# Optimization experiments

Measured on AMD Instinct MI355X. Metric: run time of the kernel, lower is better.

The kernel has to match this reference:

```python
import jax, jax.numpy as jnp
import numpy as np
from jax import lax

# ---- custom-numeric primitives matching the torch Function classes ----

def _sign1(x):
    # torch.sign with sign(0) -> 1
    return jnp.where(x >= 0, jnp.ones_like(x), -jnp.ones_like(x))

bin_act = _sign1            # BinaryActivation.forward
bin_weight = _sign1         # WeightsToBinary.forward
round_bias = jnp.round      # BiasToInt.forward

C_IN, C_OUT, K = 14, 128, 7
H_MID = 2 * K               # h = k * 2 = 14
PAD = K // 2                # 3


def _conv(x, w, b, stride, pad, groups):
    y = lax.conv_general_dilated(
        x, w,
        window_strides=(stride, stride),
        padding=((pad, pad), (pad, pad)),
        dimension_numbers=("NCHW", "OIHW", "NCHW"),
        feature_group_count=groups,
    )
    return y + b[None, :, None, None]


def setup_inputs() -> dict:
    key = jax.random.key(0)
    ks = jax.random.split(key, 7)
    B, H, W = 8, 384, 384
    x = jax.random.normal(ks[0], (B, C_IN, H, W), dtype=jnp.float32)
    # latent float weights in roughly (-1, 1) like a trained BNN
    w1 = 0.5 * jax.random.normal(ks[1], (H_MID, 1, K, K), dtype=jnp.float32)      # depthwise, groups=C_IN
    b1 = 0.5 * jax.random.normal(ks[2], (H_MID,), dtype=jnp.float32)
    w2 = 0.5 * jax.random.normal(ks[3], (C_OUT, H_MID, 1, 1), dtype=jnp.float32)
    b2 = 0.5 * jax.random.normal(ks[4], (C_OUT,), dtype=jnp.float32)
    w3 = 0.5 * jax.random.normal(ks[5], (C_OUT, C_OUT, 1, 1), dtype=jnp.float32)
    b3 = 0.5 * jax.random.normal(ks[6], (C_OUT,), dtype=jnp.float32)
    return {"x": x, "w1": w1, "b1": b1, "w2": w2, "b2": b2, "w3": w3, "b3": b3}


def reference(x, w1, b1, w2, b2, w3, b3):
    # first=True: center then binarize input
    x = bin_act(x - jnp.mean(x))
    # conv1: depthwise k x k, stride 1, padding k//2 (same spatial)
    y = bin_act(_conv(x, bin_weight(w1), round_bias(b1), 1, PAD, C_IN))
    # conv2: 1x1 conv but padding k//2 (grows spatial by 2*PAD) -- quirk of source
    y = bin_act(_conv(y, bin_weight(w2), round_bias(b2), 1, PAD, 1))
    # conv3: 1x1 conv, stride 3, padding 1
    y = bin_act(_conv(y, bin_weight(w3), round_bias(b3), 3, 1, 1))
    return y
```

## Files before the change

### kernel.cpp

```cpp
#include <hip/hip_runtime.h>
#include <hip/hip_bf16.h>

#define NB     8
#define CIN    14
#define COUT   128
#define HW     384
#define OUT_HW 131
#define P      (OUT_HW*OUT_HW)
#define ROWS   390
#define NTOT   (NB*CIN*HW*HW)
#define NROWS  (NB*CIN*ROWS)
#define NPACK  1024
#define CAND_B 0.002f
#define NSLOT  8
#define NPAIR  66

typedef unsigned long long u64;
typedef unsigned int u32;

struct PackedW {
    uint4 padz;
    uint4 ringz;
    u64   w1pack[CIN];
    int   b1i[CIN];
};

__global__ __launch_bounds__(256) void pass1(
    const float* __restrict__ x, u64* __restrict__ xbin,
    double* __restrict__ part, u64* __restrict__ cands, u32* __restrict__ ccnt,
    const float* __restrict__ w1, const float* __restrict__ b1,
    const float* __restrict__ w2, const float* __restrict__ b2,
    const float* __restrict__ w3, const float* __restrict__ b3,
    uint4* __restrict__ zlut, PackedW* __restrict__ pw)
{
    const int tid  = threadIdx.x;
    const int lane = tid & 63;
    const int wv   = tid >> 6;

    if (blockIdx.x < NPACK) {
        const u64 lmlt = (1ull << lane) - 1ull;
        double s0 = 0.0, s1 = 0.0;
        const int wid = blockIdx.x * 4 + wv;
        for (int row = wid; row < NROWS; row += NPACK * 4) {
            int nc = row / ROWS;
            int rr = row - nc * ROWS;
            int r  = rr - 3;
            u64 v = 0;
            u32 running = 0;
            u64* crow = cands + (size_t)row * NSLOT;
            if (r >= 0 && r < HW) {
                const float* xr = x + ((size_t)nc * HW + r) * HW;
                float f0 = __builtin_nontemporal_load(xr + lane);
                float f1 = __builtin_nontemporal_load(xr + 64 + lane);
                float f2 = __builtin_nontemporal_load(xr + 128 + lane);
                float f3 = __builtin_nontemporal_load(xr + 192 + lane);
                float f4 = __builtin_nontemporal_load(xr + 256 + lane);
                float f5 = __builtin_nontemporal_load(xr + 320 + lane);
                s0 += ((double)f0 + (double)f1) + (double)f2;
                s1 += ((double)f3 + (double)f4) + (double)f5;
                u64 b0 = __ballot(f0 >= 0.f);
                u64 b1_ = __ballot(f1 >= 0.f);
                u64 b2_ = __ballot(f2 >= 0.f);
                u64 b3_ = __ballot(f3 >= 0.f);
                u64 b4_ = __ballot(f4 >= 0.f);
                u64 b5_ = __ballot(f5 >= 0.f);
                v = lane == 0 ? b0 : lane == 1 ? b1_ : lane == 2 ? b2_ :
                    lane == 3 ? b3_ : lane == 4 ? b4_ : lane == 5 ? b5_ : 0;

                const u32 pbase = (u32)row * 512u + (u32)lane;
                float fq[6] = {f0, f1, f2, f3, f4, f5};
                #pragma unroll
                for (int q = 0; q < 6; q++) {
                    u64 cq = __ballot(__builtin_fabsf(fq[q]) < CAND_B);
                    if (cq) {
                        if (__builtin_fabsf(fq[q]) < CAND_B) {
                            u32 slot = running + (u32)__popcll(cq & lmlt);
                            if (slot < NSLOT)
                                crow[slot] = ((u64)__float_as_uint(fq[q]) << 32)
                                           | (pbase + (u32)q * 64u);
                        }
                        running += (u32)__popcll(cq);
                    }
                }
            }
            if (lane < 8) xbin[(size_t)row * 8 + lane] = (lane < 6) ? v : 0;
            if (lane == 0) ccnt[row] = (running > NSLOT) ? NSLOT : running;
        }
        double s = s0 + s1;
        for (int off = 32; off; off >>= 1) s += __shfl_down(s, off);
        __shared__ double wsum[4];
        if (lane == 0) wsum[wv] = s;
        __syncthreads();
        if (tid == 0) part[blockIdx.x] = ((wsum[0] + wsum[1]) + (wsum[2] + wsum[3]));
        return;
    }

    if (blockIdx.x < NPACK + 64) {
        __shared__ u32  sw2e[COUT];
        __shared__ uint4 sw3p[COUT];
        __shared__ int  st3[COUT];
        if (tid < COUT) {
            u32 wb = 0;
            const float* w2r = w2 + tid * CIN;
            for (int c = 0; c < CIN; c++) wb |= (u32)(w2r[c] >= 0.f) << c;
            int b2i = (int)rintf(b2[tid]);
            sw2e[tid] = wb | ((u32)((CIN + b2i) >> 1) << 16);
            st3[tid] = (COUT + (int)rintf(b3[tid])) >> 1;
        }
        {
            int co = tid >> 1, half = tid & 1;
            const float* wr = w3 + co * COUT + half * 64;
            u64 mm = 0;
            #pragma unroll 8
            for (int c = 0; c < 64; c++) mm |= (u64)(wr[c] >= 0.f) << c;
            if (half == 0) { sw3p[co].x = (u32)mm; sw3p[co].y = (u32)(mm >> 32); }
            else           { sw3p[co].z = (u32)mm; sw3p[co].w = (u32)(mm >> 32); }
        }
        __syncthreads();

        const u32 y1v = (blockIdx.x - NPACK) * 256 + tid;
        u64 y2lo = 0, y2hi = 0;
        #pragma unroll 8
        for (int co = 0; co < 64; co++) {
            u32 e = sw2e[co];
            int p = __popc((y1v ^ e) & 0x3FFFu);
            y2lo |= (u64)(p <= ((int)e >> 16)) << co;
        }
        #pragma unroll 8
        for (int co = 0; co < 64; co++) {
            u32 e = sw2e[64 + co];
            int p = __popc((y1v ^ e) & 0x3FFFu);
            y2hi |= (u64)(p <= ((int)e >> 16)) << co;
        }
        u32 z[4] = {0, 0, 0, 0};
        #pragma unroll 4
        for (int co = 0; co < COUT; co++) {
            uint4 w = sw3p[co];
            int pp = (int)(__popcll(y2lo ^ (((u64)w.y << 32) | w.x))
                         + __popcll(y2hi ^ (((u64)w.w << 32) | w.z)));
            z[co >> 5] |= (u32)(pp <= st3[co]) << (co & 31);
        }
        zlut[y1v] = make_uint4(z[0], z[1], z[2], z[3]);
        return;
    }

    {
        __shared__ u64 sBorder[2], sPad[2], sRing[2];
        __shared__ u64 sw3lo[COUT], sw3hi[COUT];
        __shared__ int sb3[COUT];
        if (tid < COUT) {
            const float* wr = w3 + tid * COUT;
            u64 lo = 0, hi = 0;
            #pragma unroll 8
            for (int c = 0; c < 64; c++) lo |= (u64)(wr[c] >= 0.f) << c;
            #pragma unroll 8
            for (int c = 0; c < 64; c++) hi |= (u64)(wr[64 + c] >= 0.f) << c;
            sw3lo[tid] = lo; sw3hi[tid] = hi;
            int b2i = (int)rintf(b2[tid]);
            int b3i = (int)rintf(b3[tid]);
            sb3[tid] = b3i;
            u64 bb2 = __ballot(b2i >= 0);
            u64 bb3 = __ballot(b3i >= 0);
            if (lane == 0) { sBorder[wv] = bb2; sPad[wv] = bb3; }
        } else {
            int q = tid - COUT;
            if (q < CIN) {
                const float* wr = w1 + q * 49;
                u64 pk = 0;
                for (int c = 0; c < 49; c++) pk |= (u64)(wr[c] >= 0.f) << c;
                pw->w1pack[q] = pk;
                pw->b1i[q] = (int)rintf(b1[q]);
            }
        }
        __syncthreads();
        if (tid < COUT) {
            int s3 = COUT + sb3[tid]
                   - 2 * (int)(__popcll(sBorder[0] ^ sw3lo[tid]) + __popcll(sBorder[1] ^ sw3hi[tid]));
            u64 rb = __ballot(s3 >= 0);
            if (lane == 0) sRing[wv] = rb;
        }
        __syncthreads();
        if (tid == 0) {
            pw->padz  = make_uint4((u32)sPad[0],  (u32)(sPad[0] >> 32),  (u32)sPad[1],  (u32)(sPad[1] >> 32));
            pw->ringz = make_uint4((u32)sRing[0], (u32)(sRing[0] >> 32), (u32)sRing[1], (u32)(sRing[1] >> 32));
        }
    }
}

__global__ __launch_bounds__(256) void bnn_row(
    const u64* __restrict__ xbin, const PackedW* __restrict__ pw,
    const uint4* __restrict__ zlut, const double* __restrict__ part,
    const u64* __restrict__ cands, const u32* __restrict__ ccnt,
    float* __restrict__ out)
{
    __shared__ u64 xrows[CIN][10][8];
    __shared__ u32 zl[4][2][132];
    __shared__ u64 sw1[CIN];
    __shared__ int sb1[CIN];
    __shared__ double wsum[4];

    const int tid  = threadIdx.x;
    const int lane = tid & 63;
    const int wv   = tid >> 6;
    const u32 blk  = blockIdx.x;
    const u32 n  = blk / NPAIR;
    const u32 ig = blk - n * NPAIR;
    const int i0 = 2 * (int)ig;
    const int nv = (i0 + 1 <= 130) ? 2 : 1;
    const bool anyInt = (ig >= 1 && ig <= 64);
    const int ps = 3 * i0 - 4;

    if (tid < CIN) { sw1[tid] = pw->w1pack[tid]; sb1[tid] = pw->b1i[tid]; }

    if (anyInt) {
        double t = 0.0;
        for (int q = tid; q < NPACK; q += 256) t += part[q];
        for (int off = 32; off; off >>= 1) t += __shfl_down(t, off);
        if (lane == 0) wsum[wv] = t;

        for (int t2 = tid; t2 < CIN * 80; t2 += 256) {
            int ci  = t2 / 80;
            int rem = t2 - ci * 80;
            int dy  = rem >> 3, w = rem & 7;
            xrows[ci][dy][w] =
                xbin[(((size_t)n * CIN + ci) * ROWS + (u32)(ps + dy)) * 8 + w];
        }
    }
    __syncthreads();

    if (anyInt) {
        const float m = (float)((((wsum[0] + wsum[1]) + (wsum[2] + wsum[3]))
                                 / (double)NTOT));
        if (tid < CIN * 10) {
            int ci = tid / 10, dy = tid - ci * 10;
            u32 gr = ((u32)n * CIN + (u32)ci) * ROWS + (u32)(ps + dy);
            u32 cnt = ccnt[gr];
            for (u32 s = 0; s < cnt; s++) {
                u64 e = cands[(size_t)gr * NSLOT + s];
                float v = __uint_as_float((u32)(e >> 32));
                bool bz = (v >= 0.f), bm = (v >= m);
                if (bz != bm) {
                    u32 pos = (u32)e;
                    xrows[ci][dy][(pos >> 6) & 7] ^= 1ull << (pos & 63);
                }
            }
        }
    }
    __syncthreads();

    for (int t = tid; t < nv * OUT_HW; t += 256) {
        const int di = (t >= OUT_HW) ? 1 : 0;
        const int j  = t - di * OUT_HW;
        const int i  = i0 + di;
        const bool interiorI = (i >= 2 && i <= 129);
        uint4 zz;
        if (i == 0 || j == 0) {
            zz = pw->padz;
        } else if (!interiorI || j == 1 || j == 130) {
            zz = pw->ringz;
        } else {
            const int p0 = 3 * i - 4;
            const int c0 = 3 * j - 7;
            const int lsh = (c0 < 0) ? 1 : 0;
            const int c0c = (c0 < 0) ? 0 : c0;
            const int k   = c0c >> 6;
            const int off = c0c & 63;
            const u64 selz = off ? ~0ull : 0ull;
            const int shl1 = (64 - off) & 63;
            u32 vm = 0x7Fu;
            if (c0 < 0)    vm = 0x7Eu;
            if (c0 == 380) vm = 0x0Fu;
            u64 vmrep = (u64)vm * 0x0000040810204081ull;
            u64 rmask = (1ull << 49) - 1;
            if (p0 < 3)   rmask &= ~((1ull << (7 * (3 - p0))) - 1);
            if (p0 > 380) rmask &= (1ull << (7 * (387 - p0))) - 1;
            const u64 M = vmrep & rmask;
            const int npop = (int)__popcll(M);
            const int dyb = 3 * di;

            u32 y1v = 0;
            #pragma unroll
            for (int ci = 0; ci < CIN; ci++) {
                u64 bits = 0;
                #pragma unroll
                for (int dy = 0; dy < 7; dy++) {
                    u64 w0 = xrows[ci][dyb + dy][k];
                    u64 w1 = xrows[ci][dyb + dy][k + 1];
                    u64 v = (w0 >> off) | ((w1 & selz) << shl1);
                    u32 b7 = ((u32)v << lsh) & 0x7Fu;
                    bits |= (u64)b7 << (7 * dy);
                }
                int T = sb1[ci] + npop - 2 * (int)__popcll((bits ^ sw1[ci]) & M);
                y1v |= (u32)(T >= 0) << ci;
            }
            zz = zlut[y1v];
        }
        zl[0][di][j] = zz.x; zl[1][di][j] = zz.y;
        zl[2][di][j] = zz.z; zl[3][di][j] = zz.w;
    }
    __syncthreads();

    const size_t base = (size_t)n * COUT * P + (size_t)i0 * OUT_HW;
    const int tot = nv * OUT_HW;
    for (int co = wv; co < COUT; co += 4) {
        const u32 b = co & 31;
        const u32* zp = &zl[co >> 5][0][0];
        float* op = out + base + (size_t)co * P;
        for (int t = lane; t < tot; t += 64) {
            const int di = (t >= OUT_HW) ? 1 : 0;
            const int j  = t - di * OUT_HW;
            u32 w = zp[di * 132 + j];
            op[t] = ((w >> b) & 1u) ? 1.0f : -1.0f;
        }
    }
}

extern "C" void kernel_launch(void* const* d_in, const int* in_sizes, int n_in,
                              void* d_out, int out_size, void* d_ws, size_t ws_size,
                              hipStream_t stream) {
    const float* x  = (const float*)d_in[0];
    const float* w1 = (const float*)d_in[1];
    const float* b1 = (const float*)d_in[2];
    const float* w2 = (const float*)d_in[3];
    const float* b2 = (const float*)d_in[4];
    const float* w3 = (const float*)d_in[5];
    const float* b3 = (const float*)d_in[6];
    float* out = (float*)d_out;

    double*  partials = (double*)d_ws;
    PackedW* pw       = (PackedW*)((char*)d_ws + 8448);
    uint4*   zlut     = (uint4*)((char*)d_ws + 16384);
    u64*     xbin     = (u64*)((char*)d_ws + 278528);
    u64*     cands    = (u64*)((char*)d_ws + 3074048);
    u32*     ccnt     = (u32*)((char*)d_ws + 5869568);

    pass1<<<NPACK + 64 + 1, 256, 0, stream>>>(x, xbin, partials, cands, ccnt,
                                              w1, b1, w2, b2, w3, b3, zlut, pw);
    bnn_row<<<NB * NPAIR, 256, 0, stream>>>(xbin, pw, zlut, partials,
                                            cands, ccnt, out);
}
```

Baseline: 58.26 us.

## Split output expansion into separate kernel with vectorized float4 stores

The row kernel now writes the packed 128-bit channel masks per pixel to a workspace instead of expanding them into 128 float planes itself. A new unpack kernel launches four blocks per (batch, channel) plane, aligns to 16 bytes and writes the ±1 floats with float4 stores. The goal is fully coalesced, vectorized output writes across many more blocks than the original 528, so the dominant output write bandwidth is used better. The cost is an extra kernel launch and a workspace round trip of about 2.2 MB.

```diff
diff --git a/kernel.cpp b/kernel.cpp
--- a/kernel.cpp
+++ b/kernel.cpp
@@ -7,6 +7,7 @@
 #define HW     384
 #define OUT_HW 131
 #define P      (OUT_HW*OUT_HW)
+#define TOTPIX (NB*P)
 #define ROWS   390
 #define NTOT   (NB*CIN*HW*HW)
 #define NROWS  (NB*CIN*ROWS)
@@ -14,9 +15,11 @@
 #define CAND_B 0.002f
 #define NSLOT  8
 #define NPAIR  66
+#define QELT   4291
 
 typedef unsigned long long u64;
 typedef unsigned int u32;
+typedef float f4 __attribute__((ext_vector_type(4)));
 
 struct PackedW {
     uint4 padz;
@@ -187,11 +190,11 @@
     }
 }
 
-__global__ __launch_bounds__(256) void bnn_row(
+__global__ __launch_bounds__(256) void conv_z2(
     const u64* __restrict__ xbin, const PackedW* __restrict__ pw,
     const uint4* __restrict__ zlut, const double* __restrict__ part,
     const u64* __restrict__ cands, const u32* __restrict__ ccnt,
-    float* __restrict__ out)
+    u32* __restrict__ zws)
 {
     __shared__ u64 xrows[CIN][10][8];
     __shared__ u32 zl[4][2][132];
@@ -300,18 +303,56 @@
     }
     __syncthreads();
 
-    const size_t base = (size_t)n * COUT * P + (size_t)i0 * OUT_HW;
+    const u32 rbase = n * P + (u32)i0 * OUT_HW;
     const int tot = nv * OUT_HW;
-    for (int co = wv; co < COUT; co += 4) {
-        const u32 b = co & 31;
-        const u32* zp = &zl[co >> 5][0][0];
-        float* op = out + base + (size_t)co * P;
-        for (int t = lane; t < tot; t += 64) {
-            const int di = (t >= OUT_HW) ? 1 : 0;
-            const int j  = t - di * OUT_HW;
-            u32 w = zp[di * 132 + j];
-            op[t] = ((w >> b) & 1u) ? 1.0f : -1.0f;
-        }
+    for (int t = tid; t < 4 * tot; t += 256) {
+        int qq  = t / tot;
+        int rem = t - qq * tot;
+        int di  = (rem >= OUT_HW) ? 1 : 0;
+        int j   = rem - di * OUT_HW;
+        zws[(size_t)qq * TOTPIX + rbase + (u32)di * OUT_HW + j] = zl[qq][di][j];
+    }
+}
+
+__global__ __launch_bounds__(256) void unpack4(
+    const u32* __restrict__ zws, float* __restrict__ out)
+{
+    const u32 blk = blockIdx.x;
+    const u32 q   = blk >> 2;
+    const int s   = blk & 3;
+    const int tid = threadIdx.x;
+    const u32 n  = q >> 7, co = q & 127u, b = co & 31u;
+    const u32* zp = zws + (co >> 5) * TOTPIX + n * P;
+    float* op = out + (size_t)q * P;
+
+    const int lo = s * QELT;
+    const int hi = (lo + QELT < P) ? lo + QELT : P;
+    const int mis = (int)((q * (u32)P + (u32)lo) & 3u);
+    int a0 = mis ? (4 - mis) : 0;
+    if (lo + a0 > hi) a0 = hi - lo;
+
+    if (tid < a0) {
+        u32 w = zp[lo + tid];
+        op[lo + tid] = ((w >> b) & 1u) ? 1.0f : -1.0f;
+    }
+    const int start = lo + a0;
+    const int nch = (hi - start) >> 2;
+    for (int c = tid; c < nch; c += 256) {
+        int p0 = start + 4 * c;
+        u32 w0 = zp[p0], w1 = zp[p0 + 1], w2 = zp[p0 + 2], w3 = zp[p0 + 3];
+        f4 f;
+        f.x = ((w0 >> b) & 1u) ? 1.0f : -1.0f;
+        f.y = ((w1 >> b) & 1u) ? 1.0f : -1.0f;
+        f.z = ((w2 >> b) & 1u) ? 1.0f : -1.0f;
+        f.w = ((w3 >> b) & 1u) ? 1.0f : -1.0f;
+        *(f4*)(op + p0) = f;
+    }
+    const int done = start + 4 * nch;
+    const int rem  = hi - done;
+    if (tid >= 64 && tid < 64 + rem) {
+        int pix = done + (tid - 64);
+        u32 w = zp[pix];
+        op[pix] = ((w >> b) & 1u) ? 1.0f : -1.0f;
     }
 }
 
@@ -333,9 +374,11 @@
     u64*     xbin     = (u64*)((char*)d_ws + 278528);
     u64*     cands    = (u64*)((char*)d_ws + 3074048);
     u32*     ccnt     = (u32*)((char*)d_ws + 5869568);
+    u32*     zws      = (u32*)((char*)d_ws + 6045696);
 
     pass1<<<NPACK + 64 + 1, 256, 0, stream>>>(x, xbin, partials, cands, ccnt,
                                               w1, b1, w2, b2, w3, b3, zlut, pw);
-    bnn_row<<<NB * NPAIR, 256, 0, stream>>>(xbin, pw, zlut, partials,
-                                            cands, ccnt, out);
+    conv_z2<<<NB * NPAIR, 256, 0, stream>>>(xbin, pw, zlut, partials,
+                                            cands, ccnt, zws);
+    unpack4<<<NB * COUT * 4, 256, 0, stream>>>(zws, out);
 }
```

Result: no change. 57.47 us (-1.4%).
